# Performance work log

Measured on AMD Instinct MI355X. Metric: run time of the kernel, lower is better.

Reference implementation:

```python
import jax, jax.numpy as jnp
import numpy as np

D_MODEL = 1024
N_HEADS = 16
HEAD_DIM = D_MODEL // N_HEADS
SEQ = 2048
BATCH = 2
ROPE_BASE = 10000.0


def rope_cos_sin(seq_len, dim, dtype=jnp.float32):
    inv_freq = 1.0 / (ROPE_BASE ** (jnp.arange(0, dim, 2, dtype=jnp.float32) / dim))
    pos = jnp.arange(seq_len, dtype=jnp.float32)
    freqs = jnp.outer(pos, inv_freq)              # [S, dim/2]
    emb = jnp.concatenate([freqs, freqs], axis=-1)  # [S, dim]
    return jnp.cos(emb).astype(dtype), jnp.sin(emb).astype(dtype)


def rotate_half(x):
    x1, x2 = jnp.split(x, 2, axis=-1)
    return jnp.concatenate([-x2, x1], axis=-1)


def setup_inputs() -> dict:
    key = jax.random.key(0)
    kx, kq, kk, kv, ko = jax.random.split(key, 5)
    x = jax.random.normal(kx, (BATCH, SEQ, D_MODEL), dtype=jnp.float32)
    # causal boolean mask, broadcastable to [B, H, S, S]
    attn_mask = jnp.tril(jnp.ones((SEQ, SEQ), dtype=bool))[None, None]
    s = 1.0 / np.sqrt(D_MODEL)
    Wq = jax.random.normal(kq, (D_MODEL, D_MODEL), dtype=jnp.float32) * s
    Wk = jax.random.normal(kk, (D_MODEL, D_MODEL), dtype=jnp.float32) * s
    Wv = jax.random.normal(kv, (D_MODEL, D_MODEL), dtype=jnp.float32) * s
    Wo = jax.random.normal(ko, (D_MODEL, D_MODEL), dtype=jnp.float32) * s
    return {"x": x, "attn_mask": attn_mask, "Wq": Wq, "Wk": Wk, "Wv": Wv, "Wo": Wo}


def reference(x, attn_mask, Wq, Wk, Wv, Wo):
    B, S, _ = x.shape
    dtype = x.dtype
    # projections (nn.Linear: x @ W.T)
    def split_heads(t):
        return t.reshape(B, S, N_HEADS, HEAD_DIM).transpose(0, 2, 1, 3)  # [B,H,S,Dh]
    q = split_heads(x @ Wq.T)
    k = split_heads(x @ Wk.T)
    v = split_heads(x @ Wv.T)
    # RoPE
    cos, sin = rope_cos_sin(S, HEAD_DIM, dtype)  # [S, Dh]
    cos = cos[None, None]
    sin = sin[None, None]
    q = q * cos + rotate_half(q) * sin
    k = k * cos + rotate_half(k) * sin
    # float mask: 0 where True, finfo.min where False
    neg = jnp.finfo(dtype).min
    float_mask = jnp.where(attn_mask, jnp.zeros((), dtype), jnp.full((), neg, dtype))
    # scaled dot product attention
    scale = 1.0 / np.sqrt(HEAD_DIM)
    scores = jnp.einsum("bhqd,bhkd->bhqk", q, k) * scale + float_mask
    attn = jax.nn.softmax(scores, axis=-1)
    out = jnp.einsum("bhqk,bhkd->bhqd", attn, v)  # [B,H,S,Dh]
    out = out.transpose(0, 2, 1, 3).reshape(B, S, D_MODEL)
    return out @ Wo.T
```

## Files before the change

kernel.cpp:

```cpp
#include <hip/hip_runtime.h>
#include <hip/hip_bf16.h>
#include <math.h>

typedef unsigned short ushort_t;
typedef __attribute__((ext_vector_type(8))) short short8;
typedef __attribute__((ext_vector_type(4))) float f32x4;

#define D_MODEL 1024
#define SEQ     2048
#define NH      16
#define HD      64
#define BATCH   2
#define M_TOTAL (BATCH * SEQ)
#define SCL     0.18033688f
#define HSZ     4194304

__device__ __forceinline__ ushort_t f2bf(float f) {
    __hip_bfloat16 h = __float2bfloat16(f);
    ushort_t u;
    __builtin_memcpy(&u, &h, 2);
    return u;
}
__device__ __forceinline__ unsigned pack2(float a, float b) {
    __hip_bfloat162 h = __float22bfloat162_rn(make_float2(a, b));
    unsigned u;
    __builtin_memcpy(&u, &h, 4);
    return u;
}
__device__ __forceinline__ float fexp2(float x) { return __builtin_amdgcn_exp2f(x); }

typedef const __attribute__((address_space(1))) void* gp_t;
typedef __attribute__((address_space(3))) void* lp_t;
__device__ __forceinline__ void cp16(const void* g, void* l) {
    __builtin_amdgcn_global_load_lds((gp_t)g, (lp_t)l, 16, 0, 0);
}

__global__ __launch_bounds__(256) void prep(
    const float* __restrict__ x,
    const float* __restrict__ w0, const float* __restrict__ w1,
    const float* __restrict__ w2, const float* __restrict__ w3,
    ushort_t* __restrict__ xb, ushort_t* __restrict__ wb,
    float2* __restrict__ tab)
{
    int bid = blockIdx.x;
    if (bid < 4096) {
        size_t e = ((size_t)bid * 256 + threadIdx.x) * 8;
        const float* src;
        ushort_t* dst;
        size_t off;
        if (e < (size_t)HSZ) {
            src = x; dst = xb; off = e;
        } else {
            size_t r = e - HSZ;
            int j = (int)(r >> 20);
            off = r & 1048575u;
            src = (j == 0) ? w0 : (j == 1) ? w1 : (j == 2) ? w2 : w3;
            dst = wb + ((size_t)j << 20);
        }
        float4 a = *(const float4*)&src[off];
        float4 b = *(const float4*)&src[off + 4];
        uint4 u;
        u.x = pack2(a.x, a.y);
        u.y = pack2(a.z, a.w);
        u.z = pack2(b.x, b.y);
        u.w = pack2(b.z, b.w);
        *(uint4*)&dst[off] = u;
    } else {
        int idx = (bid - 4096) * 256 + threadIdx.x;
        int i = idx & 31, s = idx >> 5;
        float invf = powf(10000.0f, -(float)(2 * i) * (1.0f / 64.0f));
        float fr = (float)s * invf;
        float sn, cs;
        sincosf(fr, &sn, &cs);
        tab[idx] = make_float2(cs, sn);
    }
}


#define STAGE(K0, SB) do {                                                   \
    cp16(&A [(size_t)(m0 + ro0) * K + (K0) + c0 * 8], &As[SB][i0 * 8]);      \
    cp16(&A [(size_t)(m0 + ro1) * K + (K0) + c1 * 8], &As[SB][i1 * 8]);      \
    cp16(&Wp[(size_t)(n0 + ro0) * K + (K0) + c0 * 8], &Bs[SB][i0 * 8]);      \
    if constexpr (BN == 128) {                                               \
        cp16(&Wp[(size_t)(n0 + ro1) * K + (K0) + c1 * 8], &Bs[SB][i1 * 8]);  \
    }                                                                        \
} while (0)

#define K_ITER(SK0, BUF, SBUF, DOSTAGE, LAST) {                              \
    if constexpr (LAST) {                                                    \
        asm volatile("s_waitcnt vmcnt(0)" ::: "memory");                     \
    } else if constexpr (OMODE == 1) {                                       \
        asm volatile("s_waitcnt vmcnt(3)" ::: "memory");                     \
    } else {                                                                 \
        asm volatile("s_waitcnt vmcnt(4)" ::: "memory");                     \
    }                                                                        \
    __builtin_amdgcn_s_barrier();                                            \
    if constexpr (DOSTAGE) { STAGE(SK0, SBUF); }                             \
    short8 af_[4], bf_[NJ];                                                  \
    _Pragma("unroll")                                                        \
    for (int i = 0; i < 4; ++i) {                                            \
        int R = wm + 16 * i + r15;                                           \
        af_[i] = *(const short8*)&As[BUF][(R * 4 + ((q4 + (R >> 1)) & 3)) * 8]; \
    }                                                                        \
    _Pragma("unroll")                                                        \
    for (int j = 0; j < NJ; ++j) {                                           \
        int R = wn + 16 * j + r15;                                           \
        bf_[j] = *(const short8*)&Bs[BUF][(R * 4 + ((q4 + (R >> 1)) & 3)) * 8]; \
    }                                                                        \
    __builtin_amdgcn_s_setprio(1);                                           \
    _Pragma("unroll")                                                        \
    for (int i = 0; i < 4; ++i) {                                            \
        _Pragma("unroll")                                                    \
        for (int j = 0; j < NJ; ++j)                                         \
            acc[i][j] = __builtin_amdgcn_mfma_f32_16x16x32_bf16(             \
                af_[i], bf_[j], acc[i][j], 0, 0, 0);                         \
    }                                                                        \
    __builtin_amdgcn_s_setprio(0);                                           \
    asm volatile("s_waitcnt lgkmcnt(0)" ::: "memory");                       \
    __builtin_amdgcn_s_barrier();                                            \
}

template <int OMODE>
__global__ __launch_bounds__(256, 3) void gemm_k(
    const ushort_t* __restrict__ A,
    const ushort_t* __restrict__ W0, const ushort_t* __restrict__ W1,
    const ushort_t* __restrict__ W2,
    void* __restrict__ D0v, void* __restrict__ D1v, void* __restrict__ D2v,
    const float2* __restrict__ tab)
{
    constexpr int BN = (OMODE == 1) ? 64 : 128;
    constexpr int NJ = BN / 32;
    __shared__ ushort_t As[3][128 * 32];
    __shared__ ushort_t Bs[3][BN * 32];
    const int K = D_MODEL;
    const int t = threadIdx.x;
    const int l = t & 63, w = t >> 6;
    const int wm = (w & 1) * 64, wn = (w >> 1) * (BN / 2);
    const int r15 = l & 15, q4 = l >> 4;

    const int bid = blockIdx.x;
    const int xcd = bid & 7, loc = bid >> 3;
    const int mt = (xcd >> 1) * 8 + (loc & 7);
    int nt, z;
    if (OMODE == 0) {
        int rest = loc >> 3;
        nt = (xcd & 1) * 4 + (rest & 3);
        z  = rest >> 2;
    } else {
        nt = (xcd & 1) * 8 + (loc >> 3);
        z  = 0;
    }
    const int m0 = mt * 128, n0 = nt * BN;
    const ushort_t* Wp = (z == 0) ? W0 : (z == 1 ? W1 : W2);
    void* Dp           = (z == 0) ? D0v : (z == 1 ? D1v : D2v);

    f32x4 acc[4][NJ];
#pragma unroll
    for (int i = 0; i < 4; ++i)
#pragma unroll
        for (int j = 0; j < NJ; ++j) acc[i][j] = (f32x4){0.f, 0.f, 0.f, 0.f};

    const int i0 = t, i1 = t + 256;
    const int ro0 = i0 >> 2, c0 = ((i0 & 3) - (ro0 >> 1)) & 3;
    const int ro1 = i1 >> 2, c1 = ((i1 & 3) - (ro1 >> 1)) & 3;

    STAGE(0, 0);
    STAGE(32, 1);
#pragma unroll 1
    for (int kb = 0; kb < 10; ++kb) {
        const int k6 = kb * 96;
        K_ITER(k6 + 64,  0, 2, 1, 0)
        K_ITER(k6 + 96,  1, 0, 1, 0)
        K_ITER(k6 + 128, 2, 1, 1, 0)
    }
    K_ITER(0, 0, 0, 0, 0)
    K_ITER(0, 1, 0, 0, 1)

    if (OMODE == 1) {
        float* Dst = (float*)Dp;
#pragma unroll
        for (int i = 0; i < 4; ++i)
#pragma unroll
            for (int j = 0; j < NJ; ++j)
#pragma unroll
                for (int r = 0; r < 4; ++r) {
                    int row = m0 + wm + 16 * i + q4 * 4 + r;
                    int col = n0 + wn + 16 * j + r15;
                    Dst[(size_t)row * D_MODEL + col] = acc[i][j][r];
                }
    } else if (z < 2) {
        ushort_t* Dst = (ushort_t*)Dp;
        const float scl = (z == 0) ? SCL : 1.0f;
#pragma unroll
        for (int i = 0; i < 4; ++i) {
#pragma unroll
            for (int r = 0; r < 4; ++r) {
                int row = m0 + wm + 16 * i + q4 * 4 + r;
                int b = row >> 11, s = row & (SEQ - 1);
                const float2* trow = &tab[s * 32];
#pragma unroll
                for (int j = 0; j < 2; ++j) {
                    int col = n0 + wn + 16 * j + r15;
                    int h = col >> 6, f = 16 * j + r15;
                    float2 csn = trow[f];
                    float cs = csn.x * scl, sn = csn.y * scl;
                    float lo = acc[i][j][r], hi = acc[i][j + 2][r];
                    size_t o = (((size_t)(b * NH + h)) * SEQ + s) * HD + f;
                    Dst[o]      = f2bf(lo * cs - hi * sn);
                    Dst[o + 32] = f2bf(hi * cs + lo * sn);
                }
            }
        }
    } else {
        ushort_t* Dst = (ushort_t*)Dp;
#pragma unroll
        for (int i = 0; i < 4; ++i)
#pragma unroll
            for (int j = 0; j < 4; ++j) {
                int row0 = m0 + wm + 16 * i + q4 * 4;
                int col  = n0 + wn + 16 * j + r15;
                int b = row0 >> 11, s0 = row0 & (SEQ - 1);
                int h = col >> 6, d = col & (HD - 1);
                size_t o = (((size_t)(b * NH + h)) * HD + d) * SEQ + s0;
                uint2 u;
                u.x = pack2(acc[i][j][0], acc[i][j][1]);
                u.y = pack2(acc[i][j][2], acc[i][j][3]);
                *(uint2*)&Dst[o] = u;
            }
    }
}

#undef K_ITER
#undef STAGE

__global__ __launch_bounds__(256, 3) void attn_fused(
    const ushort_t* __restrict__ Qw, const ushort_t* __restrict__ Kw,
    const ushort_t* __restrict__ Vt, ushort_t* __restrict__ Ow)
{
    __shared__ __align__(16) ushort_t Kl[2][64 * 64];
    __shared__ __align__(16) ushort_t Vl[2][64 * 64];
    __shared__ __align__(16) ushort_t Ps[4][16 * 72];

    const int t = threadIdx.x;
    const int l = t & 63, w = t >> 6;
    const int r15 = l & 15, q4 = l >> 4;
    const int bid = blockIdx.x;
    const int loc = bid >> 3;
    const int bh  = (bid & 7) * 4 + (loc & 3);
    const int s   = 31 - (loc >> 2);
    const int m   = s * 4 + w;
    const size_t baseQK = (size_t)bh * SEQ * HD;
    const size_t baseV  = (size_t)bh * HD * SEQ;

    const int L0 = t, L1 = t + 256;
    const int r0 = L0 >> 3, c0 = (L0 & 7) ^ (r0 & 7);
    const int r1 = L1 >> 3, c1 = (L1 & 7) ^ (r1 & 7);

    const ushort_t* qp = &Qw[baseQK + (size_t)(m * 16 + r15) * HD + q4 * 8];
    short8 qf0 = *(const short8*)qp;
    short8 qf1 = *(const short8*)(qp + 32);

    f32x4 oacc[4];
    float part[4];
#pragma unroll
    for (int nb = 0; nb < 4; ++nb) oacc[nb] = (f32x4){0.f, 0.f, 0.f, 0.f};
#pragma unroll
    for (int r = 0; r < 4; ++r) part[r] = 0.f;

    const int ig0 = m * 16 + q4 * 4;
    ushort_t* ps = &Ps[w][0];

    auto stage = [&](int jt, int buf) {
        cp16(&Kw[baseQK + (size_t)(jt * 64 + r0) * HD + c0 * 8], &Kl[buf][L0 * 8]);
        cp16(&Kw[baseQK + (size_t)(jt * 64 + r1) * HD + c1 * 8], &Kl[buf][L1 * 8]);
        cp16(&Vt[baseV + (size_t)r0 * SEQ + jt * 64 + c0 * 8],   &Vl[buf][L0 * 8]);
        cp16(&Vt[baseV + (size_t)r1 * SEQ + jt * 64 + c1 * 8],   &Vl[buf][L1 * 8]);
    };

    auto process = [&](int jt, int buf) {
        f32x4 sc[4];
#pragma unroll
        for (int nb = 0; nb < 4; ++nb) {
            int R  = nb * 16 + r15;
            int a0 = R * 8 + (q4 ^ (R & 7));
            int a1 = R * 8 + ((q4 + 4) ^ (R & 7));
            short8 kb0 = *(const short8*)&Kl[buf][a0 * 8];
            short8 kb1 = *(const short8*)&Kl[buf][a1 * 8];
            f32x4 zz = (f32x4){0.f, 0.f, 0.f, 0.f};
            zz = __builtin_amdgcn_mfma_f32_16x16x32_bf16(qf0, kb0, zz, 0, 0, 0);
            sc[nb] = __builtin_amdgcn_mfma_f32_16x16x32_bf16(qf1, kb1, zz, 0, 0, 0);
        }
        const bool diag = (jt == s);
#pragma unroll
        for (int r = 0; r < 4; ++r) {
            float p0 = fexp2(sc[0][r]), p1 = fexp2(sc[1][r]);
            float p2 = fexp2(sc[2][r]), p3 = fexp2(sc[3][r]);
            if (diag) {
                int qg = ig0 + r, jb = jt * 64 + r15;
                p0 = (jb      <= qg) ? p0 : 0.f;
                p1 = (jb + 16 <= qg) ? p1 : 0.f;
                p2 = (jb + 32 <= qg) ? p2 : 0.f;
                p3 = (jb + 48 <= qg) ? p3 : 0.f;
            }
            part[r] += (p0 + p1) + (p2 + p3);
            int ro = (q4 * 4 + r) * 72 + r15;
            ps[ro]      = f2bf(p0);
            ps[ro + 16] = f2bf(p1);
            ps[ro + 32] = f2bf(p2);
            ps[ro + 48] = f2bf(p3);
        }
        short8 pf0 = *(const short8*)&ps[r15 * 72 + q4 * 8];
        short8 pf1 = *(const short8*)&ps[r15 * 72 + q4 * 8 + 32];
#pragma unroll
        for (int nb = 0; nb < 4; ++nb) {
            int R  = nb * 16 + r15;
            int a0 = R * 8 + (q4 ^ (R & 7));
            int a1 = R * 8 + ((q4 + 4) ^ (R & 7));
            short8 vb0 = *(const short8*)&Vl[buf][a0 * 8];
            short8 vb1 = *(const short8*)&Vl[buf][a1 * 8];
            f32x4 o = __builtin_amdgcn_mfma_f32_16x16x32_bf16(pf0, vb0, oacc[nb], 0, 0, 0);
            oacc[nb] = __builtin_amdgcn_mfma_f32_16x16x32_bf16(pf1, vb1, o, 0, 0, 0);
        }
    };

    stage(0, 0);
    for (int jt = 0; jt <= s; ++jt) {
        __syncthreads();
        if (jt < s) stage(jt + 1, (jt + 1) & 1);
        process(jt, jt & 1);
    }

    float lsum[4];
#pragma unroll
    for (int r = 0; r < 4; ++r) {
        float rs = part[r];
#pragma unroll
        for (int off = 1; off < 16; off <<= 1)
            rs += __shfl_xor(rs, off, 64);
        lsum[r] = 1.0f / rs;
    }

    const int b = bh >> 4, h = bh & 15;
#pragma unroll
    for (int nb = 0; nb < 4; ++nb) {
#pragma unroll
        for (int r = 0; r < 4; ++r) {
            int sg = m * 16 + q4 * 4 + r;
            int d  = nb * 16 + r15;
            Ow[((size_t)(b * SEQ + sg)) * D_MODEL + h * HD + d] =
                f2bf(oacc[nb][r] * lsum[r]);
        }
    }
}

extern "C" void kernel_launch(void* const* d_in, const int* in_sizes, int n_in,
                              void* d_out, int out_size, void* d_ws, size_t ws_size,
                              hipStream_t stream)
{
    const float* x  = (const float*)d_in[0];
    const float* Wq = (const float*)d_in[2];
    const float* Wk = (const float*)d_in[3];
    const float* Wv = (const float*)d_in[4];
    const float* Wo = (const float*)d_in[5];

    ushort_t* qw = (ushort_t*)d_ws;
    ushort_t* kw = qw + HSZ;
    ushort_t* vt = kw + HSZ;
    ushort_t* xb = vt + HSZ;
    ushort_t* aw = xb;
    ushort_t* wb = xb + HSZ;
    float2*  tab = (float2*)(wb + HSZ);

    prep<<<4096 + 256, 256, 0, stream>>>(x, Wq, Wk, Wv, Wo, xb, wb, tab);
    gemm_k<0><<<768, 256, 0, stream>>>(
        xb, wb, wb + (1 << 20), wb + (2 << 20), qw, kw, vt, tab);
    attn_fused<<<1024, 256, 0, stream>>>(qw, kw, vt, aw);
    gemm_k<1><<<512, 256, 0, stream>>>(
        aw, wb + (3 << 20), nullptr, nullptr,
        (float*)d_out, nullptr, nullptr, nullptr);
}
```

Before: 181.1 us.

## Split output-projection GEMM into dedicated kernel with BK=64 tiles and XOR swizzle

Result: no change. 177.6 us (-1.9%).

```diff
diff --git a/kernel.cpp b/kernel.cpp
--- a/kernel.cpp
+++ b/kernel.cpp
@@ -81,29 +81,25 @@
     cp16(&A [(size_t)(m0 + ro0) * K + (K0) + c0 * 8], &As[SB][i0 * 8]);      \
     cp16(&A [(size_t)(m0 + ro1) * K + (K0) + c1 * 8], &As[SB][i1 * 8]);      \
     cp16(&Wp[(size_t)(n0 + ro0) * K + (K0) + c0 * 8], &Bs[SB][i0 * 8]);      \
-    if constexpr (BN == 128) {                                               \
-        cp16(&Wp[(size_t)(n0 + ro1) * K + (K0) + c1 * 8], &Bs[SB][i1 * 8]);  \
-    }                                                                        \
+    cp16(&Wp[(size_t)(n0 + ro1) * K + (K0) + c1 * 8], &Bs[SB][i1 * 8]);      \
 } while (0)
 
 #define K_ITER(SK0, BUF, SBUF, DOSTAGE, LAST) {                              \
     if constexpr (LAST) {                                                    \
         asm volatile("s_waitcnt vmcnt(0)" ::: "memory");                     \
-    } else if constexpr (OMODE == 1) {                                       \
-        asm volatile("s_waitcnt vmcnt(3)" ::: "memory");                     \
     } else {                                                                 \
         asm volatile("s_waitcnt vmcnt(4)" ::: "memory");                     \
     }                                                                        \
     __builtin_amdgcn_s_barrier();                                            \
     if constexpr (DOSTAGE) { STAGE(SK0, SBUF); }                             \
-    short8 af_[4], bf_[NJ];                                                  \
+    short8 af_[4], bf_[4];                                                   \
     _Pragma("unroll")                                                        \
     for (int i = 0; i < 4; ++i) {                                            \
         int R = wm + 16 * i + r15;                                           \
         af_[i] = *(const short8*)&As[BUF][(R * 4 + ((q4 + (R >> 1)) & 3)) * 8]; \
     }                                                                        \
     _Pragma("unroll")                                                        \
-    for (int j = 0; j < NJ; ++j) {                                           \
+    for (int j = 0; j < 4; ++j) {                                            \
         int R = wn + 16 * j + r15;                                           \
         bf_[j] = *(const short8*)&Bs[BUF][(R * 4 + ((q4 + (R >> 1)) & 3)) * 8]; \
     }                                                                        \
@@ -111,7 +107,7 @@
     _Pragma("unroll")                                                        \
     for (int i = 0; i < 4; ++i) {                                            \
         _Pragma("unroll")                                                    \
-        for (int j = 0; j < NJ; ++j)                                         \
+        for (int j = 0; j < 4; ++j)                                          \
             acc[i][j] = __builtin_amdgcn_mfma_f32_16x16x32_bf16(             \
                 af_[i], bf_[j], acc[i][j], 0, 0, 0);                         \
     }                                                                        \
@@ -120,45 +116,36 @@
     __builtin_amdgcn_s_barrier();                                            \
 }
 
-template <int OMODE>
-__global__ __launch_bounds__(256, 3) void gemm_k(
+__global__ __launch_bounds__(256, 3) void gemm_qkv(
     const ushort_t* __restrict__ A,
     const ushort_t* __restrict__ W0, const ushort_t* __restrict__ W1,
     const ushort_t* __restrict__ W2,
     void* __restrict__ D0v, void* __restrict__ D1v, void* __restrict__ D2v,
     const float2* __restrict__ tab)
 {
-    constexpr int BN = (OMODE == 1) ? 64 : 128;
-    constexpr int NJ = BN / 32;
     __shared__ ushort_t As[3][128 * 32];
-    __shared__ ushort_t Bs[3][BN * 32];
+    __shared__ ushort_t Bs[3][128 * 32];
     const int K = D_MODEL;
     const int t = threadIdx.x;
     const int l = t & 63, w = t >> 6;
-    const int wm = (w & 1) * 64, wn = (w >> 1) * (BN / 2);
+    const int wm = (w & 1) * 64, wn = (w >> 1) * 64;
     const int r15 = l & 15, q4 = l >> 4;
 
     const int bid = blockIdx.x;
     const int xcd = bid & 7, loc = bid >> 3;
     const int mt = (xcd >> 1) * 8 + (loc & 7);
-    int nt, z;
-    if (OMODE == 0) {
-        int rest = loc >> 3;
-        nt = (xcd & 1) * 4 + (rest & 3);
-        z  = rest >> 2;
-    } else {
-        nt = (xcd & 1) * 8 + (loc >> 3);
-        z  = 0;
-    }
-    const int m0 = mt * 128, n0 = nt * BN;
+    int rest = loc >> 3;
+    const int nt = (xcd & 1) * 4 + (rest & 3);
+    const int z  = rest >> 2;
+    const int m0 = mt * 128, n0 = nt * 128;
     const ushort_t* Wp = (z == 0) ? W0 : (z == 1 ? W1 : W2);
     void* Dp           = (z == 0) ? D0v : (z == 1 ? D1v : D2v);
 
-    f32x4 acc[4][NJ];
+    f32x4 acc[4][4];
 #pragma unroll
     for (int i = 0; i < 4; ++i)
 #pragma unroll
-        for (int j = 0; j < NJ; ++j) acc[i][j] = (f32x4){0.f, 0.f, 0.f, 0.f};
+        for (int j = 0; j < 4; ++j) acc[i][j] = (f32x4){0.f, 0.f, 0.f, 0.f};
 
     const int i0 = t, i1 = t + 256;
     const int ro0 = i0 >> 2, c0 = ((i0 & 3) - (ro0 >> 1)) & 3;
@@ -176,19 +163,7 @@
     K_ITER(0, 0, 0, 0, 0)
     K_ITER(0, 1, 0, 0, 1)
 
-    if (OMODE == 1) {
-        float* Dst = (float*)Dp;
-#pragma unroll
-        for (int i = 0; i < 4; ++i)
-#pragma unroll
-            for (int j = 0; j < NJ; ++j)
-#pragma unroll
-                for (int r = 0; r < 4; ++r) {
-                    int row = m0 + wm + 16 * i + q4 * 4 + r;
-                    int col = n0 + wn + 16 * j + r15;
-                    Dst[(size_t)row * D_MODEL + col] = acc[i][j][r];
-                }
-    } else if (z < 2) {
+    if (z < 2) {
         ushort_t* Dst = (ushort_t*)Dp;
         const float scl = (z == 0) ? SCL : 1.0f;
 #pragma unroll
@@ -233,6 +208,117 @@
 #undef K_ITER
 #undef STAGE
 
+
+#define STAGE_O(K0, SB) do {                                                 \
+    cp16(&A [(size_t)(m0 + roa0) * K + (K0) + ca0 * 8], &As[SB][ia0 * 8]);   \
+    cp16(&A [(size_t)(m0 + roa1) * K + (K0) + ca1 * 8], &As[SB][ia1 * 8]);   \
+    cp16(&A [(size_t)(m0 + roa2) * K + (K0) + ca2 * 8], &As[SB][ia2 * 8]);   \
+    cp16(&A [(size_t)(m0 + roa3) * K + (K0) + ca3 * 8], &As[SB][ia3 * 8]);   \
+    cp16(&Wp[(size_t)(n0 + rob0) * K + (K0) + cb0 * 8], &Bs[SB][ib0 * 8]);   \
+    cp16(&Wp[(size_t)(n0 + rob1) * K + (K0) + cb1 * 8], &Bs[SB][ib1 * 8]);   \
+} while (0)
+
+#define K_ITER_O(SK0, BUF, SBUF, DOSTAGE, LAST) {                            \
+    if constexpr (LAST) {                                                    \
+        asm volatile("s_waitcnt vmcnt(0)" ::: "memory");                     \
+    } else {                                                                 \
+        asm volatile("s_waitcnt vmcnt(6)" ::: "memory");                     \
+    }                                                                        \
+    __builtin_amdgcn_s_barrier();                                            \
+    if constexpr (DOSTAGE) { STAGE_O(SK0, SBUF); }                           \
+    short8 af_[4][2], bf_[2][2];                                             \
+    _Pragma("unroll")                                                        \
+    for (int i = 0; i < 4; ++i) {                                            \
+        int R = wm + 16 * i + r15;                                           \
+        _Pragma("unroll")                                                    \
+        for (int kk = 0; kk < 2; ++kk)                                       \
+            af_[i][kk] = *(const short8*)                                    \
+                &As[BUF][(R * 8 + ((kk * 4 + q4) ^ (R & 7))) * 8];           \
+    }                                                                        \
+    _Pragma("unroll")                                                        \
+    for (int j = 0; j < 2; ++j) {                                            \
+        int R = wn + 16 * j + r15;                                           \
+        _Pragma("unroll")                                                    \
+        for (int kk = 0; kk < 2; ++kk)                                       \
+            bf_[j][kk] = *(const short8*)                                    \
+                &Bs[BUF][(R * 8 + ((kk * 4 + q4) ^ (R & 7))) * 8];           \
+    }                                                                        \
+    __builtin_amdgcn_s_setprio(1);                                           \
+    _Pragma("unroll")                                                        \
+    for (int kk = 0; kk < 2; ++kk) {                                         \
+        _Pragma("unroll")                                                    \
+        for (int i = 0; i < 4; ++i) {                                        \
+            _Pragma("unroll")                                                \
+            for (int j = 0; j < 2; ++j)                                      \
+                acc[i][j] = __builtin_amdgcn_mfma_f32_16x16x32_bf16(         \
+                    af_[i][kk], bf_[j][kk], acc[i][j], 0, 0, 0);             \
+        }                                                                    \
+    }                                                                        \
+    __builtin_amdgcn_s_setprio(0);                                           \
+    asm volatile("s_waitcnt lgkmcnt(0)" ::: "memory");                       \
+    __builtin_amdgcn_s_barrier();                                            \
+}
+
+__global__ __launch_bounds__(256, 2) void gemm_o(
+    const ushort_t* __restrict__ A, const ushort_t* __restrict__ Wp,
+    float* __restrict__ Dst)
+{
+    __shared__ ushort_t As[3][128 * 64];
+    __shared__ ushort_t Bs[3][64 * 64];
+    const int K = D_MODEL;
+    const int t = threadIdx.x;
+    const int l = t & 63, w = t >> 6;
+    const int wm = (w & 1) * 64, wn = (w >> 1) * 32;
+    const int r15 = l & 15, q4 = l >> 4;
+
+    const int bid = blockIdx.x;
+    const int xcd = bid & 7, loc = bid >> 3;
+    const int mt = (xcd >> 1) * 8 + (loc & 7);
+    const int nt = (xcd & 1) * 8 + (loc >> 3);
+    const int m0 = mt * 128, n0 = nt * 64;
+
+    f32x4 acc[4][2];
+#pragma unroll
+    for (int i = 0; i < 4; ++i)
+#pragma unroll
+        for (int j = 0; j < 2; ++j) acc[i][j] = (f32x4){0.f, 0.f, 0.f, 0.f};
+
+    const int ia0 = t,       roa0 = ia0 >> 3, ca0 = (ia0 & 7) ^ (roa0 & 7);
+    const int ia1 = t + 256, roa1 = ia1 >> 3, ca1 = (ia1 & 7) ^ (roa1 & 7);
+    const int ia2 = t + 512, roa2 = ia2 >> 3, ca2 = (ia2 & 7) ^ (roa2 & 7);
+    const int ia3 = t + 768, roa3 = ia3 >> 3, ca3 = (ia3 & 7) ^ (roa3 & 7);
+    const int ib0 = t,       rob0 = ib0 >> 3, cb0 = (ib0 & 7) ^ (rob0 & 7);
+    const int ib1 = t + 256, rob1 = ib1 >> 3, cb1 = (ib1 & 7) ^ (rob1 & 7);
+
+    STAGE_O(0, 0);
+    STAGE_O(64, 1);
+#pragma unroll 1
+    for (int kb = 0; kb < 4; ++kb) {
+        const int k6 = kb * 192;
+        K_ITER_O(k6 + 128, 0, 2, 1, 0)
+        K_ITER_O(k6 + 192, 1, 0, 1, 0)
+        K_ITER_O(k6 + 256, 2, 1, 1, 0)
+    }
+    K_ITER_O(896, 0, 2, 1, 0)
+    K_ITER_O(960, 1, 0, 1, 0)
+    K_ITER_O(0,   2, 0, 0, 0)
+    K_ITER_O(0,   0, 0, 0, 1)
+
+#pragma unroll
+    for (int i = 0; i < 4; ++i)
+#pragma unroll
+        for (int j = 0; j < 2; ++j)
+#pragma unroll
+            for (int r = 0; r < 4; ++r) {
+                int row = m0 + wm + 16 * i + q4 * 4 + r;
+                int col = n0 + wn + 16 * j + r15;
+                Dst[(size_t)row * D_MODEL + col] = acc[i][j][r];
+            }
+}
+
+#undef K_ITER_O
+#undef STAGE_O
+
 __global__ __launch_bounds__(256, 3) void attn_fused(
     const ushort_t* __restrict__ Qw, const ushort_t* __restrict__ Kw,
     const ushort_t* __restrict__ Vt, ushort_t* __restrict__ Ow)
@@ -279,6 +365,7 @@
 
     auto process = [&](int jt, int buf) {
         f32x4 sc[4];
+        __builtin_amdgcn_s_setprio(1);
 #pragma unroll
         for (int nb = 0; nb < 4; ++nb) {
             int R  = nb * 16 + r15;
@@ -290,6 +377,7 @@
             zz = __builtin_amdgcn_mfma_f32_16x16x32_bf16(qf0, kb0, zz, 0, 0, 0);
             sc[nb] = __builtin_amdgcn_mfma_f32_16x16x32_bf16(qf1, kb1, zz, 0, 0, 0);
         }
+        __builtin_amdgcn_s_setprio(0);
         const bool diag = (jt == s);
 #pragma unroll
         for (int r = 0; r < 4; ++r) {
@@ -311,6 +399,7 @@
         }
         short8 pf0 = *(const short8*)&ps[r15 * 72 + q4 * 8];
         short8 pf1 = *(const short8*)&ps[r15 * 72 + q4 * 8 + 32];
+        __builtin_amdgcn_s_setprio(1);
 #pragma unroll
         for (int nb = 0; nb < 4; ++nb) {
             int R  = nb * 16 + r15;
@@ -321,6 +410,7 @@
             f32x4 o = __builtin_amdgcn_mfma_f32_16x16x32_bf16(pf0, vb0, oacc[nb], 0, 0, 0);
             oacc[nb] = __builtin_amdgcn_mfma_f32_16x16x32_bf16(pf1, vb1, o, 0, 0, 0);
         }
+        __builtin_amdgcn_s_setprio(0);
     };
 
     stage(0, 0);
@@ -372,10 +462,8 @@
     float2*  tab = (float2*)(wb + HSZ);
 
     prep<<<4096 + 256, 256, 0, stream>>>(x, Wq, Wk, Wv, Wo, xb, wb, tab);
-    gemm_k<0><<<768, 256, 0, stream>>>(
+    gemm_qkv<<<768, 256, 0, stream>>>(
         xb, wb, wb + (1 << 20), wb + (2 << 20), qw, kw, vt, tab);
     attn_fused<<<1024, 256, 0, stream>>>(qw, kw, vt, aw);
-    gemm_k<1><<<512, 256, 0, stream>>>(
-        aw, wb + (3 << 20), nullptr, nullptr,
-        (float*)d_out, nullptr, nullptr, nullptr);
-}
+    gemm_o<<<512, 256, 0, stream>>>(aw, wb + (3 << 20), (float*)d_out);
+}
```
